# Kernel optimization log

Hardware: AMD Instinct MI355X
Metric: run time of the kernel (lower is better)

The kernel has to match this reference:

```python
import jax, jax.numpy as jnp
import numpy as np

IN_FEATURES = [32, 32]
OUT_FEATURES = [64, 64]
RANKS = [16, 16, 16, 16]


def _make_cores(key):
    dims = IN_FEATURES + OUT_FEATURES
    ranks = RANKS
    # init scale as in the torch module
    var = 2 ** (1.0 / len(dims)) / np.prod(np.power(np.array(ranks) + np.array(IN_FEATURES + IN_FEATURES), 1.0 / len(dims)))
    ub = float(np.sqrt(3.0 * var))
    ranks_ext = [ranks[-1]] + list(ranks)
    cores = []
    for i in range(len(dims)):
        key, k = jax.random.split(key)
        cores.append(jax.random.uniform(k, (ranks_ext[i], dims[i], ranks_ext[i + 1]), jnp.float32, -ub, ub))
    return cores, key


def setup_inputs() -> dict:
    key = jax.random.key(0)
    cores, key = _make_cores(key)
    key, kx, kb = jax.random.split(key, 3)
    x = jax.random.normal(kx, (8192, int(np.prod(IN_FEATURES))), jnp.float32)
    bias = jax.random.normal(kb, (int(np.prod(OUT_FEATURES)),), jnp.float32)
    return {"x": x, "core0": cores[0], "core1": cores[1], "core2": cores[2], "core3": cores[3], "bias": bias}


def reference(x, core0, core1, core2, core3, bias):
    # Tensor-ring contraction to build the dense weight, then linear.
    # core shapes: (16,32,16), (16,32,16), (16,64,16), (16,64,16)
    w = jnp.tensordot(core0, core1, axes=([2], [0]))        # (r, i0, i1, r)
    w = jnp.tensordot(w, core2, axes=([3], [0]))            # (r, i0, i1, o0, r)
    # last core: contract w's trailing rank with core axis 0 AND w's leading
    # rank with core's trailing rank (closes the ring) -> (i0, i1, o0, o1)
    w = jnp.tensordot(w, core3, axes=([4, 0], [0, 2]))
    d_out = int(np.prod(OUT_FEATURES))
    w = w.reshape(d_out, -1)                                # (4096, 1024)
    return x @ w.T + bias
```

## Files before the change

### kernel.cpp

```cpp
#include <hip/hip_runtime.h>
#include <hip/hip_bf16.h>
#include <stdint.h>

typedef unsigned short ushort_t;
typedef __attribute__((ext_vector_type(8))) short short8;
typedef __attribute__((ext_vector_type(4))) float floatx4;

__device__ __forceinline__ ushort_t f2bf(float f) {
    union { float f; unsigned u; } v; v.f = f;
    unsigned r = v.u + 0x7fffu + ((v.u >> 16) & 1u);
    return (ushort_t)(r >> 16);
}

__device__ __forceinline__ void async16(ushort_t* lds, const ushort_t* g) {
    __builtin_amdgcn_global_load_lds(
        (const __attribute__((address_space(1))) unsigned int*)g,
        (__attribute__((address_space(3))) unsigned int*)lds, 16, 0, 0);
}

__global__ __launch_bounds__(256) void prep_all(const float* __restrict__ x,
                                                const float* __restrict__ c0,
                                                const float* __restrict__ c1,
                                                const float* __restrict__ c2,
                                                const float* __restrict__ c3,
                                                ushort_t* __restrict__ Xb,
                                                ushort_t* __restrict__ A2b,
                                                ushort_t* __restrict__ B2t) {
    const int b = blockIdx.x, t = threadIdx.x;
    if (b < 8192) {
        int i = b * 256 + t;
        float4 v = ((const float4*)x)[i];
        ushort4 r;
        r.x = f2bf(v.x); r.y = f2bf(v.y); r.z = f2bf(v.z); r.w = f2bf(v.w);
        ((ushort4*)Xb)[i] = r;
    } else if (b < 9216) {
        int id = (b - 8192) * 256 + t;
        int k = id & 255, ii = id >> 8;
        int r0 = k >> 4, r2 = k & 15;
        int i0 = ii >> 5, i1 = ii & 31;
        const float* p0 = c0 + (r0 * 32 + i0) * 16;
        const float* p1 = c1 + i1 * 16 + r2;
        float s = 0.f;
#pragma unroll
        for (int r1 = 0; r1 < 16; r1++) s += p0[r1] * p1[r1 * 512];
        A2b[id] = f2bf(s);
    } else {
        int id = (b - 9216) * 256 + t;
        int k = id & 255, oo = id >> 8;
        int r0 = k >> 4, r2 = k & 15;
        int o0 = oo >> 6, o1 = oo & 63;
        const float* p2 = c2 + (r2 * 64 + o0) * 16;
        const float* p3 = c3 + o1 * 16 + r0;
        float s = 0.f;
#pragma unroll
        for (int r3 = 0; r3 < 16; r3++) s += p2[r3] * p3[r3 * 1024];
        B2t[id] = f2bf(s);
    }
}

__global__ __launch_bounds__(256) void build_w_mfma(const ushort_t* __restrict__ A2b,
                                                    const ushort_t* __restrict__ B2t,
                                                    ushort_t* __restrict__ W) {
    __shared__ ushort_t As[128 * 32];
    __shared__ ushort_t Bs[128 * 32];
    const int t = threadIdx.x;
    const int row0 = blockIdx.x * 128;
    const int col0 = blockIdx.y * 128;
    const int w = t >> 6, l = t & 63;
    const int wm = w >> 1, wn = w & 1;
    const int quad = l >> 4, ln = l & 15;

    floatx4 acc[4][4] = {};

    const ushort_t* aSrc = A2b + (size_t)(row0 + (t >> 2)) * 256 + (t & 3) * 8;
    const ushort_t* bSrc = B2t + (size_t)(col0 + (t >> 2)) * 256 + (t & 3) * 8;

    for (int kk = 0; kk < 256; kk += 32) {
        async16(&As[t * 8],        aSrc + kk);
        async16(&As[2048 + t * 8], aSrc + 64 * 256 + kk);
        async16(&Bs[t * 8],        bSrc + kk);
        async16(&Bs[2048 + t * 8], bSrc + 64 * 256 + kk);
        __syncthreads();

        short8 a[4], b[4];
#pragma unroll
        for (int ti = 0; ti < 4; ti++)
            a[ti] = *(const short8*)&As[(wm * 64 + ti * 16 + ln) * 32 + quad * 8];
#pragma unroll
        for (int tj = 0; tj < 4; tj++)
            b[tj] = *(const short8*)&Bs[(wn * 64 + tj * 16 + ln) * 32 + quad * 8];
#pragma unroll
        for (int ti = 0; ti < 4; ti++)
#pragma unroll
            for (int tj = 0; tj < 4; tj++)
                acc[ti][tj] = __builtin_amdgcn_mfma_f32_16x16x32_bf16(
                    a[ti], b[tj], acc[ti][tj], 0, 0, 0);
        __syncthreads();
    }

#pragma unroll
    for (int tj = 0; tj < 4; tj++) {
        const int n = col0 + wn * 64 + tj * 16 + ln;
#pragma unroll
        for (int ti = 0; ti < 4; ti++) {
            const int m = row0 + wm * 64 + ti * 16 + quad * 4;
#pragma unroll
            for (int r = 0; r < 4; r++)
                W[(size_t)(m + r) * 4096 + n] = f2bf(acc[ti][tj][r]);
        }
    }
}

__global__ __launch_bounds__(256) void gemm_bt_bias(const ushort_t* __restrict__ Xb,
                                                    const ushort_t* __restrict__ Wb,
                                                    const float* __restrict__ bias,
                                                    float* __restrict__ out) {
    __shared__ ushort_t As[128 * 32];
    __shared__ ushort_t Bs[128 * 32];
    const int t = threadIdx.x;
    const int row0 = blockIdx.x * 128;
    const int col0 = blockIdx.y * 128;
    const int w = t >> 6, l = t & 63;
    const int wm = w >> 1, wn = w & 1;
    const int quad = l >> 4, ln = l & 15;

    floatx4 acc[4][4] = {};

    const ushort_t* aSrc = Xb + (size_t)(row0 + (t >> 2)) * 1024 + (t & 3) * 8;
    const ushort_t* bSrc = Wb + (size_t)(col0 + (t >> 2)) * 1024 + (t & 3) * 8;

    for (int kk = 0; kk < 1024; kk += 32) {
        async16(&As[t * 8],        aSrc + kk);
        async16(&As[2048 + t * 8], aSrc + 64 * 1024 + kk);
        async16(&Bs[t * 8],        bSrc + kk);
        async16(&Bs[2048 + t * 8], bSrc + 64 * 1024 + kk);
        __syncthreads();

        short8 a[4], b[4];
#pragma unroll
        for (int ti = 0; ti < 4; ti++)
            a[ti] = *(const short8*)&As[(wm * 64 + ti * 16 + ln) * 32 + quad * 8];
#pragma unroll
        for (int tj = 0; tj < 4; tj++)
            b[tj] = *(const short8*)&Bs[(wn * 64 + tj * 16 + ln) * 32 + quad * 8];
#pragma unroll
        for (int ti = 0; ti < 4; ti++)
#pragma unroll
            for (int tj = 0; tj < 4; tj++)
                acc[ti][tj] = __builtin_amdgcn_mfma_f32_16x16x32_bf16(
                    a[ti], b[tj], acc[ti][tj], 0, 0, 0);
        __syncthreads();
    }

#pragma unroll
    for (int tj = 0; tj < 4; tj++) {
        const int n = col0 + wn * 64 + tj * 16 + ln;
        const float bv = bias[n];
#pragma unroll
        for (int ti = 0; ti < 4; ti++) {
            const int m = row0 + wm * 64 + ti * 16 + quad * 4;
            float* o = out + (size_t)m * 4096 + n;
#pragma unroll
            for (int r = 0; r < 4; r++)
                o[(size_t)r * 4096] = acc[ti][tj][r] + bv;
        }
    }
}

extern "C" void kernel_launch(void* const* d_in, const int* in_sizes, int n_in,
                              void* d_out, int out_size, void* d_ws, size_t ws_size,
                              hipStream_t stream) {
    const float* x    = (const float*)d_in[0];
    const float* c0   = (const float*)d_in[1];
    const float* c1   = (const float*)d_in[2];
    const float* c2   = (const float*)d_in[3];
    const float* c3   = (const float*)d_in[4];
    const float* bias = (const float*)d_in[5];
    float* out = (float*)d_out;

    char* ws = (char*)d_ws;
    ushort_t* Xb  = (ushort_t*)ws;
    ushort_t* Wb  = (ushort_t*)(ws + (16u << 20));
    ushort_t* A2b = (ushort_t*)(ws + (24u << 20));
    ushort_t* B2t = (ushort_t*)(ws + (25u << 20));

    hipLaunchKernelGGL(prep_all, dim3(13312), dim3(256), 0, stream,
                       x, c0, c1, c2, c3, Xb, A2b, B2t);
    hipLaunchKernelGGL(build_w_mfma, dim3(8, 32), dim3(256), 0, stream, A2b, B2t, Wb);
    hipLaunchKernelGGL(gemm_bt_bias, dim3(64, 32), dim3(256), 0, stream, Xb, Wb, bias, out);
}
```

Before: 251.7 us.

## Replace dense weight build with factored two-stage tensor-ring contraction

Drops the materialised 4096x1024 weight. x is first contracted with a per-output-block factor (Bg1) into an intermediate U of shape 8192x1024. A second GEMM then contracts U with A2 along the rank dimension and writes the output with the bias added, using float4 stores. The goal is to cut the FLOPs of the full 8192x1024x4096 GEMM by exploiting low-rank structure, which also brings workgroup swizzling and reuses the output buffer as scratch for Xb. The costs are an extra bf16 rounding of U and a second GEMM whose MFMA shape has poor reuse (one B fragment per K step).

```diff
diff --git a/kernel.cpp b/kernel.cpp
--- a/kernel.cpp
+++ b/kernel.cpp
@@ -25,7 +25,7 @@
                                                 const float* __restrict__ c3,
                                                 ushort_t* __restrict__ Xb,
                                                 ushort_t* __restrict__ A2b,
-                                                ushort_t* __restrict__ B2t) {
+                                                ushort_t* __restrict__ Bg1) {
     const int b = blockIdx.x, t = threadIdx.x;
     if (b < 8192) {
         int i = b * 256 + t;
@@ -46,88 +46,37 @@
         A2b[id] = f2bf(s);
     } else {
         int id = (b - 9216) * 256 + t;
-        int k = id & 255, oo = id >> 8;
+        int c = id & 1023, n = id >> 10;
+        int bq = n >> 8, k = n & 255;
         int r0 = k >> 4, r2 = k & 15;
-        int o0 = oo >> 6, o1 = oo & 63;
+        int o0 = bq * 16 + (c >> 6), o1 = c & 63;
         const float* p2 = c2 + (r2 * 64 + o0) * 16;
         const float* p3 = c3 + o1 * 16 + r0;
         float s = 0.f;
 #pragma unroll
         for (int r3 = 0; r3 < 16; r3++) s += p2[r3] * p3[r3 * 1024];
-        B2t[id] = f2bf(s);
-    }
-}
-
-__global__ __launch_bounds__(256) void build_w_mfma(const ushort_t* __restrict__ A2b,
-                                                    const ushort_t* __restrict__ B2t,
-                                                    ushort_t* __restrict__ W) {
+        Bg1[id] = f2bf(s);
+    }
+}
+
+__global__ __launch_bounds__(256) void gemm1_u(const ushort_t* __restrict__ Xb,
+                                               const ushort_t* __restrict__ Bg1,
+                                               ushort_t* __restrict__ U) {
     __shared__ ushort_t As[128 * 32];
     __shared__ ushort_t Bs[128 * 32];
     const int t = threadIdx.x;
-    const int row0 = blockIdx.x * 128;
-    const int col0 = blockIdx.y * 128;
+    const unsigned orig = blockIdx.x;
+    const unsigned wg = (orig & 7) * 64 + (orig >> 3);
+    const int row0 = (int)(wg >> 3) * 128;
+    const int col0 = (int)(wg & 7) * 128;
     const int w = t >> 6, l = t & 63;
     const int wm = w >> 1, wn = w & 1;
     const int quad = l >> 4, ln = l & 15;
 
     floatx4 acc[4][4] = {};
 
-    const ushort_t* aSrc = A2b + (size_t)(row0 + (t >> 2)) * 256 + (t & 3) * 8;
-    const ushort_t* bSrc = B2t + (size_t)(col0 + (t >> 2)) * 256 + (t & 3) * 8;
-
-    for (int kk = 0; kk < 256; kk += 32) {
-        async16(&As[t * 8],        aSrc + kk);
-        async16(&As[2048 + t * 8], aSrc + 64 * 256 + kk);
-        async16(&Bs[t * 8],        bSrc + kk);
-        async16(&Bs[2048 + t * 8], bSrc + 64 * 256 + kk);
-        __syncthreads();
-
-        short8 a[4], b[4];
-#pragma unroll
-        for (int ti = 0; ti < 4; ti++)
-            a[ti] = *(const short8*)&As[(wm * 64 + ti * 16 + ln) * 32 + quad * 8];
-#pragma unroll
-        for (int tj = 0; tj < 4; tj++)
-            b[tj] = *(const short8*)&Bs[(wn * 64 + tj * 16 + ln) * 32 + quad * 8];
-#pragma unroll
-        for (int ti = 0; ti < 4; ti++)
-#pragma unroll
-            for (int tj = 0; tj < 4; tj++)
-                acc[ti][tj] = __builtin_amdgcn_mfma_f32_16x16x32_bf16(
-                    a[ti], b[tj], acc[ti][tj], 0, 0, 0);
-        __syncthreads();
-    }
-
-#pragma unroll
-    for (int tj = 0; tj < 4; tj++) {
-        const int n = col0 + wn * 64 + tj * 16 + ln;
-#pragma unroll
-        for (int ti = 0; ti < 4; ti++) {
-            const int m = row0 + wm * 64 + ti * 16 + quad * 4;
-#pragma unroll
-            for (int r = 0; r < 4; r++)
-                W[(size_t)(m + r) * 4096 + n] = f2bf(acc[ti][tj][r]);
-        }
-    }
-}
-
-__global__ __launch_bounds__(256) void gemm_bt_bias(const ushort_t* __restrict__ Xb,
-                                                    const ushort_t* __restrict__ Wb,
-                                                    const float* __restrict__ bias,
-                                                    float* __restrict__ out) {
-    __shared__ ushort_t As[128 * 32];
-    __shared__ ushort_t Bs[128 * 32];
-    const int t = threadIdx.x;
-    const int row0 = blockIdx.x * 128;
-    const int col0 = blockIdx.y * 128;
-    const int w = t >> 6, l = t & 63;
-    const int wm = w >> 1, wn = w & 1;
-    const int quad = l >> 4, ln = l & 15;
-
-    floatx4 acc[4][4] = {};
-
-    const ushort_t* aSrc = Xb + (size_t)(row0 + (t >> 2)) * 1024 + (t & 3) * 8;
-    const ushort_t* bSrc = Wb + (size_t)(col0 + (t >> 2)) * 1024 + (t & 3) * 8;
+    const ushort_t* aSrc = Xb  + (size_t)(row0 + (t >> 2)) * 1024 + (t & 3) * 8;
+    const ushort_t* bSrc = Bg1 + (size_t)(col0 + (t >> 2)) * 1024 + (t & 3) * 8;
 
     for (int kk = 0; kk < 1024; kk += 32) {
         async16(&As[t * 8],        aSrc + kk);
@@ -155,14 +104,82 @@
 #pragma unroll
     for (int tj = 0; tj < 4; tj++) {
         const int n = col0 + wn * 64 + tj * 16 + ln;
-        const float bv = bias[n];
 #pragma unroll
         for (int ti = 0; ti < 4; ti++) {
             const int m = row0 + wm * 64 + ti * 16 + quad * 4;
-            float* o = out + (size_t)m * 4096 + n;
 #pragma unroll
             for (int r = 0; r < 4; r++)
-                o[(size_t)r * 4096] = acc[ti][tj][r] + bv;
+                U[(size_t)(m + r) * 1024 + n] = f2bf(acc[ti][tj][r]);
+        }
+    }
+}
+
+__global__ __launch_bounds__(256) void gemm2_tr(const ushort_t* __restrict__ U,
+                                                const ushort_t* __restrict__ A2b,
+                                                const float* __restrict__ bias,
+                                                float* __restrict__ out) {
+    __shared__ ushort_t Us[4 * 128 * 32];
+    __shared__ ushort_t A2s[32 * 264];
+    const int t = threadIdx.x;
+    const unsigned orig = blockIdx.x;
+    const unsigned wg = (orig & 7) * 256 + (orig >> 3);
+    const int jt = (int)(wg & 31), mt = (int)(wg >> 5);
+    const int row0 = mt * 128;
+    const int a0 = jt * 32;
+    const int w = t >> 6, l = t & 63;
+    const int wm = w >> 1, wn = w & 1;
+    const int quad = l >> 4, ln = l & 15;
+
+    {
+        const int r = t >> 3, cb = t & 7;
+#pragma unroll
+        for (int s = 0; s < 4; s++) {
+            int ch = cb + s * 8;
+            short8 v = *(const short8*)&A2b[(size_t)(a0 + r) * 256 + ch * 8];
+            *(short8*)&A2s[r * 264 + ch * 8] = v;
+        }
+    }
+
+    floatx4 acc[4][4] = {};
+
+    const ushort_t* uSrc = U + (size_t)(row0 + (t >> 2)) * 1024 + (t & 3) * 8;
+
+    for (int kk = 0; kk < 256; kk += 32) {
+#pragma unroll
+        for (int b = 0; b < 4; b++) {
+            async16(&Us[b * 4096 + t * 8],        uSrc + b * 256 + kk);
+            async16(&Us[b * 4096 + 2048 + t * 8], uSrc + 64 * 1024 + b * 256 + kk);
+        }
+        __syncthreads();
+
+        short8 bfrag = *(const short8*)&A2s[(wn * 16 + ln) * 264 + kk + quad * 8];
+#pragma unroll
+        for (int b = 0; b < 4; b++) {
+            short8 au[4];
+#pragma unroll
+            for (int ti = 0; ti < 4; ti++)
+                au[ti] = *(const short8*)&Us[b * 4096 + (wm * 64 + ti * 16 + ln) * 32 + quad * 8];
+#pragma unroll
+            for (int ti = 0; ti < 4; ti++)
+                acc[b][ti] = __builtin_amdgcn_mfma_f32_16x16x32_bf16(
+                    au[ti], bfrag, acc[b][ti], 0, 0, 0);
+        }
+        __syncthreads();
+    }
+
+    const int a = a0 + wn * 16 + ln;
+    const float4 bv = ((const float4*)bias)[a];
+#pragma unroll
+    for (int ti = 0; ti < 4; ti++) {
+        const int m = row0 + wm * 64 + ti * 16 + quad * 4;
+#pragma unroll
+        for (int r = 0; r < 4; r++) {
+            float4 o;
+            o.x = acc[0][ti][r] + bv.x;
+            o.y = acc[1][ti][r] + bv.y;
+            o.z = acc[2][ti][r] + bv.z;
+            o.w = acc[3][ti][r] + bv.w;
+            *(float4*)&out[(size_t)(m + r) * 4096 + (size_t)a * 4] = o;
         }
     }
 }
@@ -179,13 +196,13 @@
     float* out = (float*)d_out;
 
     char* ws = (char*)d_ws;
-    ushort_t* Xb  = (ushort_t*)ws;
-    ushort_t* Wb  = (ushort_t*)(ws + (16u << 20));
-    ushort_t* A2b = (ushort_t*)(ws + (24u << 20));
-    ushort_t* B2t = (ushort_t*)(ws + (25u << 20));
+    ushort_t* Xb  = (ushort_t*)out;
+    ushort_t* U   = (ushort_t*)ws;
+    ushort_t* A2b = (ushort_t*)(ws + (16u << 20));
+    ushort_t* Bg1 = (ushort_t*)(ws + (17u << 20));
 
     hipLaunchKernelGGL(prep_all, dim3(13312), dim3(256), 0, stream,
-                       x, c0, c1, c2, c3, Xb, A2b, B2t);
-    hipLaunchKernelGGL(build_w_mfma, dim3(8, 32), dim3(256), 0, stream, A2b, B2t, Wb);
-    hipLaunchKernelGGL(gemm_bt_bias, dim3(64, 32), dim3(256), 0, stream, Xb, Wb, bias, out);
-}
+                       x, c0, c1, c2, c3, Xb, A2b, Bg1);
+    hipLaunchKernelGGL(gemm1_u, dim3(512), dim3(256), 0, stream, Xb, Bg1, U);
+    hipLaunchKernelGGL(gemm2_tr, dim3(2048), dim3(256), 0, stream, U, A2b, bias, out);
+}
```

New measurement: 256.5 us. Within noise of the previous version (+1.9%).
